# Kernel tuning notes

Hardware: AMD Instinct MI355X
Metric: run time of the kernel (lower is better)

Reference implementation:

```python
import jax, jax.numpy as jnp
import numpy as np
from math import factorial as _fact

# ---- sizes / hyperparams (match init_kwargs) ----
N_NODES, N_EDGES = 8192, 131072
C, H, NRAD, NUM_LAYERS = 64, 64, 8, 2
R_MAX, AVG_NN = 5.0, 16.0
LS = (0, 1, 2)  # irreps degrees carried by node features and edge SH

# ---- real-basis Clebsch-Gordan coefficients (computed once in numpy) ----
def _cg_scalar(j1, m1, j2, m2, j3, m3):
    if m1 + m2 != m3:
        return 0.0
    pre = ((2*j3+1) * _fact(j1+j2-j3) * _fact(j1-j2+j3) * _fact(-j1+j2+j3)
           / _fact(j1+j2+j3+1)) ** 0.5
    pre *= (_fact(j1+m1)*_fact(j1-m1)*_fact(j2+m2)*_fact(j2-m2)
            * _fact(j3+m3)*_fact(j3-m3)) ** 0.5
    s = 0.0
    for k in range(max(0, j2-j3-m1, j1+m2-j3), min(j1+j2-j3, j1-m1, j2+m2)+1):
        s += (-1)**k / (_fact(k)*_fact(j1+j2-j3-k)*_fact(j1-m1-k)
                        * _fact(j2+m2-k)*_fact(j3-j2+m1+k)*_fact(j3-j1-m2+k))
    return pre * s

def _U_real(l):
    # unitary: Y_real = U @ Y_complex, components ordered m=-l..l
    U = np.zeros((2*l+1, 2*l+1), dtype=complex)
    s2 = 2 ** -0.5
    for m in range(-l, l+1):
        if m > 0:
            U[m+l, m+l] = (-1)**m * s2
            U[m+l, -m+l] = s2
        elif m == 0:
            U[l, l] = 1.0
        else:
            U[m+l, m+l] = 1j*s2
            U[m+l, -m+l] = -1j*(-1)**(-m)*s2
    return U

def _real_cg(l1, l2, l3):
    Cc = np.zeros((2*l1+1, 2*l2+1, 2*l3+1))
    for i1, m1 in enumerate(range(-l1, l1+1)):
        for i2, m2 in enumerate(range(-l2, l2+1)):
            m3 = m1 + m2
            if abs(m3) <= l3:
                Cc[i1, i2, m3+l3] = _cg_scalar(l1, m1, l2, m2, l3, m3)
    U1, U2, U3 = _U_real(l1), _U_real(l2), _U_real(l3)
    W = np.einsum('ia,jb,kc,abc->ijk', U1.conj(), U2.conj(), U3, Cc.astype(complex))
    W = W.real if np.linalg.norm(W.real) >= np.linalg.norm(W.imag) else W.imag
    W = W / np.linalg.norm(W) * (2*l3+1) ** 0.5  # component-style normalization
    return jnp.asarray(W, dtype=jnp.float32)

PATHS = [(l1, l2, l3) for l1 in LS for l2 in LS for l3 in LS
         if abs(l1 - l2) <= l3 <= l1 + l2]  # 15 tensor-product paths
CGS = [_real_cg(*p) for p in PATHS]
N_PATHS = len(PATHS)


def _sph(u):
    # real spherical harmonics of unit vectors, l=0,1,2, m=-l..l ordering
    x, y, z = u[:, 0], u[:, 1], u[:, 2]
    sh0 = jnp.ones((u.shape[0], 1), u.dtype)
    sh1 = jnp.sqrt(3.0) * jnp.stack([y, z, x], axis=-1)
    sh2 = jnp.stack([jnp.sqrt(15.0)*x*y, jnp.sqrt(15.0)*y*z,
                     jnp.sqrt(5.0)/2*(3*z*z - 1.0),
                     jnp.sqrt(15.0)*x*z, jnp.sqrt(15.0)/2*(x*x - y*y)], axis=-1)
    return (sh0, sh1, sh2)


def _forward(positions, embed, w_proj, mlp_w1, mlp_b1, mlp_w2, mlp_b2, mlp_w3,
             lin_self, gate_w, gate_b, species, senders, receivers):
    n = positions.shape[0]
    rel = (positions[receivers] - positions[senders]) / R_MAX  # [E,3]
    d = jnp.linalg.norm(rel, axis=-1)                          # [E]
    u = rel / jnp.maximum(d, 1e-6)[:, None]
    sh = _sph(u)
    freqs = jnp.arange(1, NRAD + 1, dtype=positions.dtype)
    xr = jnp.clip(d, 1e-4, 1.0)[:, None]
    basis = jnp.sqrt(2.0) * jnp.sin(freqs * jnp.pi * xr) / xr  # Bessel [E,NRAD]
    cut = 0.5 * (jnp.cos(jnp.pi * jnp.clip(d, 0.0, 1.0)) + 1.0)  # smooth cutoff

    # initial species embedding -> scalar (0e) features; l>0 start at zero
    x0 = embed[species] @ w_proj                                # [N,C]
    feats = [x0[:, :, None],
             jnp.zeros((n, C, 3), x0.dtype),
             jnp.zeros((n, C, 5), x0.dtype)]

    inv_sqrt_nn = 1.0 / jnp.sqrt(jnp.asarray(AVG_NN, x0.dtype))
    for i in range(NUM_LAYERS):
        # radial MLP -> per-path, per-channel edge weights
        h = jax.nn.silu(basis @ mlp_w1[i] + mlp_b1[i])
        h = jax.nn.silu(h @ mlp_w2[i] + mlp_b2[i])
        w = (h @ mlp_w3[i]).reshape(-1, N_PATHS, C) * cut[:, None, None]
        xg = [feats[l][senders] for l in LS]                    # edge gather
        msgs = [0.0, 0.0, 0.0]
        for p, (l1, l2, l3) in enumerate(PATHS):
            m = jnp.einsum('eci,ej,ijk->eck', xg[l1], sh[l2], CGS[p])
            msgs[l3] = msgs[l3] + m * w[:, p, :, None]
        agg = [jax.ops.segment_sum(msgs[l], receivers, num_segments=n) * inv_sqrt_nn
               for l in LS]
        # self-interaction linears + gated nonlinearity + skip
        y = [jnp.einsum('ncm,cd->ndm', agg[l], lin_self[i, l]) for l in LS]
        feats[0] = feats[0] + jax.nn.silu(y[0])
        g_in = feats[0][:, :, 0]                                # [N,C] scalars
        for l in (1, 2):
            g = jax.nn.sigmoid(g_in @ gate_w[i, l-1] + gate_b[i, l-1])
            feats[l] = feats[l] + g[:, :, None] * y[l]

    # alpha = 0.5 ** l per irrep, then flatten to [N, C*(1+3+5)]
    return jnp.concatenate([(feats[l] * (0.5 ** l)).reshape(n, -1) for l in LS],
                           axis=-1)


def setup_inputs() -> dict:
    key = jax.random.key(0)
    ks = jax.random.split(key, 12)
    f32 = jnp.float32
    return {
        'positions': jax.random.normal(ks[0], (N_NODES, 3), f32),
        'species': jax.random.randint(ks[1], (N_NODES,), 0, 5),
        'senders': jax.random.randint(ks[2], (N_EDGES,), 0, N_NODES),
        'receivers': jax.random.randint(ks[3], (N_EDGES,), 0, N_NODES),
        'embed': jax.random.normal(ks[4], (5, 32), f32),
        'w_proj': jax.random.normal(ks[5], (32, C), f32) / jnp.sqrt(32.0),
        'mlp_w1': jax.random.normal(ks[6], (NUM_LAYERS, NRAD, H), f32) / jnp.sqrt(float(NRAD)),
        'mlp_b1': jnp.zeros((NUM_LAYERS, H), f32),
        'mlp_w2': jax.random.normal(ks[7], (NUM_LAYERS, H, H), f32) / jnp.sqrt(float(H)),
        'mlp_b2': jnp.zeros((NUM_LAYERS, H), f32),
        'mlp_w3': jax.random.normal(ks[8], (NUM_LAYERS, H, N_PATHS * C), f32) / jnp.sqrt(float(H)),
        'lin_self': jax.random.normal(ks[9], (NUM_LAYERS, 3, C, C), f32) / jnp.sqrt(float(C)),
        'gate_w': jax.random.normal(ks[10], (NUM_LAYERS, 2, C, C), f32) / jnp.sqrt(float(C)),
        'gate_b': jnp.zeros((NUM_LAYERS, 2, C), f32),
    }


def reference(positions, species, senders, receivers, embed, w_proj, mlp_w1,
              mlp_b1, mlp_w2, mlp_b2, mlp_w3, lin_self, gate_w, gate_b):
    return _forward(positions, embed, w_proj, mlp_w1, mlp_b1, mlp_w2, mlp_b2,
                    mlp_w3, lin_self, gate_w, gate_b, species, senders, receivers)
```

## Files before the change

kernel.cpp:

```cpp
#include <hip/hip_runtime.h>
#include <cmath>
#include <algorithm>

#define N_NODES 8192
#define N_EDGES 131072
#define NPATHS 15
#define FPN 576
#define NODE_BLK 16
#define SWROW 968

typedef unsigned short ushortx;
typedef unsigned int uintx;
typedef short short8 __attribute__((ext_vector_type(8)));
typedef float f32x4 __attribute__((ext_vector_type(4)));

constexpr int PL1[NPATHS] = {0,0,0,1,1,1,1,1,1,2,2,2,2,2,2};
constexpr int PL2[NPATHS] = {0,1,2,0,1,1,1,2,2,0,1,1,2,2,2};
constexpr int PL3[NPATHS] = {0,1,2,1,0,1,2,1,2,2,1,2,0,1,2};
constexpr int CGOFF[NPATHS] = {0,1,10,35,44,53,80,125,170,245,270,315,390,415,490};
constexpr int CGTOT = 615;
constexpr int BOFF[3] = {0,1,4};

struct CGTable { float v[CGTOT]; };

namespace cgb {
struct C2 { double re, im; };
static inline C2 cmul(C2 a, C2 b){ return {a.re*b.re - a.im*b.im, a.re*b.im + a.im*b.re}; }
static double factd(int n){ double r=1.0; for (int i=2;i<=n;++i) r*=i; return r; }

static double cg_scalar(int j1,int m1,int j2,int m2,int j3,int m3){
  if (m1+m2 != m3) return 0.0;
  double pre = std::sqrt((2.0*j3+1.0)*factd(j1+j2-j3)*factd(j1-j2+j3)*factd(-j1+j2+j3)/factd(j1+j2+j3+1));
  pre *= std::sqrt(factd(j1+m1)*factd(j1-m1)*factd(j2+m2)*factd(j2-m2)*factd(j3+m3)*factd(j3-m3));
  double s = 0.0;
  int kmin = std::max(0, std::max(j2-j3-m1, j1+m2-j3));
  int kmax = std::min(j1+j2-j3, std::min(j1-m1, j2+m2));
  for (int k=kmin;k<=kmax;++k){
    double t = 1.0/(factd(k)*factd(j1+j2-j3-k)*factd(j1-m1-k)*factd(j2+m2-k)*factd(j3-j2+m1+k)*factd(j3-j1-m2+k));
    s += (k&1) ? -t : t;
  }
  return pre*s;
}

static void makeU(int l, C2 U[5][5]){
  double s2 = std::sqrt(0.5);
  for (int a=0;a<5;++a) for (int b=0;b<5;++b) U[a][b] = {0.0,0.0};
  for (int m=-l;m<=l;++m){
    if (m > 0){
      U[m+l][ m+l] = {((m&1)?-1.0:1.0)*s2, 0.0};
      U[m+l][-m+l] = {s2, 0.0};
    } else if (m == 0){
      U[l][l] = {1.0, 0.0};
    } else {
      U[m+l][ m+l] = {0.0, s2};
      U[m+l][-m+l] = {0.0, -((((-m)&1))?-1.0:1.0)*s2};
    }
  }
}
}

static CGTable build_cg_table(){
  using namespace cgb;
  CGTable t{};
  for (int p=0;p<NPATHS;++p){
    int l1=PL1[p], l2=PL2[p], l3=PL3[p];
    int n1=2*l1+1, n2=2*l2+1, n3=2*l3+1;
    double Cc[5][5][5] = {};
    for (int i1=0;i1<n1;++i1) for (int i2=0;i2<n2;++i2){
      int m1=i1-l1, m2=i2-l2, m3=m1+m2;
      if (m3 >= -l3 && m3 <= l3) Cc[i1][i2][m3+l3] = cg_scalar(l1,m1,l2,m2,l3,m3);
    }
    C2 U1[5][5], U2[5][5], U3[5][5];
    makeU(l1,U1); makeU(l2,U2); makeU(l3,U3);
    double Wre[5][5][5]={}, Wim[5][5][5]={};
    for (int i=0;i<n1;++i) for (int j=0;j<n2;++j) for (int k=0;k<n3;++k){
      double are=0.0, aim=0.0;
      for (int a=0;a<n1;++a) for (int b=0;b<n2;++b){
        int m3 = (a-l1)+(b-l2);
        if (m3 < -l3 || m3 > l3) continue;
        double cv = Cc[a][b][m3+l3];
        if (cv == 0.0) continue;
        C2 u1c = {U1[i][a].re, -U1[i][a].im};
        C2 u2c = {U2[j][b].re, -U2[j][b].im};
        C2 tt = cmul(cmul(u1c, u2c), U3[k][m3+l3]);
        are += tt.re*cv; aim += tt.im*cv;
      }
      Wre[i][j][k]=are; Wim[i][j][k]=aim;
    }
    double nr=0.0, ni=0.0;
    for (int i=0;i<n1;++i) for (int j=0;j<n2;++j) for (int k=0;k<n3;++k){
      nr += Wre[i][j][k]*Wre[i][j][k]; ni += Wim[i][j][k]*Wim[i][j][k];
    }
    bool useRe = std::sqrt(nr) >= std::sqrt(ni);
    double nrm = std::sqrt(useRe ? nr : ni);
    double scale = std::sqrt((double)n3) / nrm;
    for (int i=0;i<n1;++i) for (int j=0;j<n2;++j) for (int k=0;k<n3;++k)
      t.v[CGOFF[p] + (i*n2+j)*n3 + k] =
        (float)((useRe ? Wre[i][j][k] : Wim[i][j][k]) * scale);
  }
  return t;
}

static const CGTable& cg_table(){ static CGTable t = build_cg_table(); return t; }

__device__ __forceinline__ float siluf(float x){ return x / (1.0f + expf(-x)); }
__device__ __forceinline__ float sigmf(float x){ return 1.0f / (1.0f + expf(-x)); }
__device__ __forceinline__ ushortx f2b(float f){
  uintx u = __float_as_uint(f);
  u += 0x7fffu + ((u >> 16) & 1u);
  return (ushortx)(u >> 16);
}
__device__ __forceinline__ float b2f(ushortx b){ return __uint_as_float(((uintx)b) << 16); }

__global__ __launch_bounds__(64) void k_init(const int* __restrict__ species,
    const float* __restrict__ embed, const float* __restrict__ wproj,
    float* __restrict__ feats)
{
  const int n = blockIdx.x, c = threadIdx.x;
  const int sp = species[n];
  float acc = 0.f;
  #pragma unroll
  for (int q=0;q<32;++q) acc += embed[sp*32+q]*wproj[q*64+c];
  feats[n*FPN + c] = acc;
  #pragma unroll
  for (int j=0;j<8;++j) feats[n*FPN + 64 + j*64 + c] = 0.f;
}

__global__ __launch_bounds__(256) void k_out(const float* __restrict__ feats,
                                             float* __restrict__ out)
{
  const int n = blockIdx.x;
  for (int j = threadIdx.x; j < FPN; j += 256){
    float sc = (j < 64) ? 1.0f : ((j < 256) ? 0.5f : 0.25f);
    out[n*FPN + j] = feats[n*FPN + j] * sc;
  }
}

__global__ __launch_bounds__(256) void k_hist(const int* __restrict__ receivers,
                                              int* __restrict__ cnt)
{
  int e = blockIdx.x*256 + threadIdx.x;
  atomicAdd(&cnt[receivers[e]], 1);
}

__global__ __launch_bounds__(1024) void k_scan(const int* __restrict__ cnt,
    int* __restrict__ row_start, int* __restrict__ cursor)
{
  __shared__ int part[1024];
  const int t = threadIdx.x;
  int loc[8];
  #pragma unroll
  for (int i=0;i<8;++i) loc[i] = cnt[t*8+i];
  int sum = 0;
  #pragma unroll
  for (int i=0;i<8;++i) sum += loc[i];
  part[t] = sum;
  __syncthreads();
  for (int off=1; off<1024; off<<=1){
    int x = (t >= off) ? part[t-off] : 0;
    __syncthreads();
    part[t] += x;
    __syncthreads();
  }
  int run = (t > 0) ? part[t-1] : 0;
  #pragma unroll
  for (int i=0;i<8;++i){
    row_start[t*8+i] = run;
    cursor[t*8+i]    = run;
    run += loc[i];
  }
  if (t == 1023) row_start[8192] = run;
}

__global__ __launch_bounds__(256) void k_scatter(const int* __restrict__ receivers,
    int* __restrict__ cursor, int* __restrict__ perm)
{
  int e = blockIdx.x*256 + threadIdx.x;
  int r = receivers[e];
  int pos = atomicAdd(&cursor[r], 1);
  perm[pos] = e;
}

__global__ __launch_bounds__(256) void k_geom(const float* __restrict__ pos,
    const int* __restrict__ senders, const int* __restrict__ receivers,
    const int* __restrict__ perm,
    float* __restrict__ sh8s, float* __restrict__ d_s,
    int* __restrict__ send_s, int* __restrict__ recv_s)
{
  const int i = blockIdx.x*256 + threadIdx.x;
  const int e = perm[i];
  const int s = senders[e], r = receivers[e];
  send_s[i] = s;
  recv_s[i] = r;
  float rx = (pos[r*3+0] - pos[s*3+0]) * 0.2f;
  float ry = (pos[r*3+1] - pos[s*3+1]) * 0.2f;
  float rz = (pos[r*3+2] - pos[s*3+2]) * 0.2f;
  float d  = sqrtf(rx*rx + ry*ry + rz*rz);
  d_s[i] = d;
  float iv = 1.0f / fmaxf(d, 1e-6f);
  float x = rx*iv, y = ry*iv, z = rz*iv;
  const float s3   = 1.7320508075688772f;
  const float s15  = 3.8729833462074170f;
  const float s5h  = 1.1180339887498949f;
  const float s15h = 1.9364916731037085f;
  sh8s[i*8+0] = s3*y;
  sh8s[i*8+1] = s3*z;
  sh8s[i*8+2] = s3*x;
  sh8s[i*8+3] = s15*x*y;
  sh8s[i*8+4] = s15*y*z;
  sh8s[i*8+5] = s5h*(3.f*z*z - 1.f);
  sh8s[i*8+6] = s15*x*z;
  sh8s[i*8+7] = s15h*(x*x - y*y);
}

__global__ __launch_bounds__(256) void k_mlp(
    const float* __restrict__ d_s,
    const float* __restrict__ w1, const float* __restrict__ b1,
    const float* __restrict__ w2, const float* __restrict__ b2,
    ushortx* __restrict__ h2p)
{
  __shared__ float s_w2[4096];
  __shared__ float s_h1[4*64];
  const int tid = threadIdx.x, wv = tid>>6, lane = tid&63;
  const float PI = 3.14159265358979323846f;
  for (int i=tid;i<4096;i+=256) s_w2[i] = w2[i];
  __syncthreads();
  #pragma unroll
  for (int ee=0; ee<2; ++ee){
    const int i = blockIdx.x*8 + wv*2 + ee;
    const float d = d_s[i];
    float xr = fminf(fmaxf(d, 1e-4f), 1.0f);
    float ixr = 1.0f/xr;
    float acc = b1[lane];
    #pragma unroll
    for (int q=0;q<8;++q){
      float bs = 1.4142135623730951f * sinf((float)(q+1)*PI*xr) * ixr;
      acc = fmaf(bs, w1[q*64+lane], acc);
    }
    s_h1[wv*64+lane] = siluf(acc);
    __syncthreads();
    float acc2 = b2[lane];
    #pragma unroll
    for (int k=0;k<64;++k) acc2 = fmaf(s_h1[wv*64+k], s_w2[k*64+lane], acc2);
    float dc = fminf(fmaxf(d, 0.f), 1.f);
    float cut = 0.5f*(cosf(PI*dc) + 1.f);
    float h2 = siluf(acc2) * cut * 0.25f;
    h2p[(size_t)i*64+lane] = f2b(h2);
    __syncthreads();
  }
}

__global__ __launch_bounds__(256) void k_w3t(const float* __restrict__ w3,
                                             ushortx* __restrict__ w3t)
{
  int g = blockIdx.x*256 + threadIdx.x;
  int n = g >> 6, k = g & 63;
  w3t[g] = f2b(w3[k*960 + n]);
}

__global__ __launch_bounds__(256) void k_aggmm(
    const float* __restrict__ featsIn, float* __restrict__ featsOut,
    const ushortx* __restrict__ h2p, const ushortx* __restrict__ w3t,
    const float* __restrict__ sh8s, const int* __restrict__ send_s,
    const int* __restrict__ recv_s, const int* __restrict__ rowst,
    const float* __restrict__ lin, const float* __restrict__ gw,
    const float* __restrict__ gb, const CGTable cg)
{
  __shared__ float   s_agg[NODE_BLK*FPN];
  __shared__ ushortx s_w[16*SWROW];
  __shared__ ushortx s_a[16*72];

  const int tid  = threadIdx.x;
  const int wv   = tid >> 6;
  const int lane = tid & 63;
  const int n0   = blockIdx.x * NODE_BLK;
  const int beg  = rowst[n0];
  const int end  = rowst[n0 + NODE_BLK];

  for (int k = tid; k < NODE_BLK*FPN; k += 256) s_agg[k] = 0.f;
  __syncthreads();

  const int q = lane >> 4, mrow = lane & 15;

  for (int ebeg = beg; ebeg < end; ebeg += 16){
    {
      int er = tid >> 4, seg = tid & 15;
      int i = ebeg + er;
      if (i >= end) i = end - 1;
      *(uint2*)&s_a[er*72 + seg*4] =
        *(const uint2*)&h2p[(size_t)i*64 + seg*4];
    }
    __syncthreads();

    short8 a0 = *(const short8*)&s_a[mrow*72 +      q*8];
    short8 a1 = *(const short8*)&s_a[mrow*72 + 32 + q*8];
    #pragma unroll
    for (int nt=0; nt<15; ++nt){
      const int col = wv*240 + nt*16 + mrow;
      short8 b0 = *(const short8*)&w3t[(size_t)col*64 +      q*8];
      short8 b1 = *(const short8*)&w3t[(size_t)col*64 + 32 + q*8];
      f32x4 acc = {0.f,0.f,0.f,0.f};
      acc = __builtin_amdgcn_mfma_f32_16x16x32_bf16(a0, b0, acc, 0, 0, 0);
      acc = __builtin_amdgcn_mfma_f32_16x16x32_bf16(a1, b1, acc, 0, 0, 0);
      #pragma unroll
      for (int r=0;r<4;++r)
        s_w[(q*4+r)*SWROW + col] = f2b(acc[r]);
    }
    __syncthreads();

    #pragma unroll
    for (int ee=0; ee<4; ++ee){
      const int slot = wv*4 + ee;
      const int i = ebeg + slot;
      if (i < end){
        const int s  = send_s[i];
        const int rl = recv_s[i] - n0;
        const float* fb = featsIn + (size_t)s*FPN;
        float X[9];
        X[0] = fb[lane];
        #pragma unroll
        for (int mm=0;mm<3;++mm) X[1+mm] = fb[64  + lane*3 + mm];
        #pragma unroll
        for (int mm=0;mm<5;++mm) X[4+mm] = fb[256 + lane*5 + mm];
        float S[9];
        S[0] = 1.f;
        #pragma unroll
        for (int j=0;j<8;++j) S[1+j] = sh8s[(size_t)i*8+j];
        float w[NPATHS];
        #pragma unroll
        for (int p=0;p<NPATHS;++p) w[p] = b2f(s_w[slot*SWROW + p*64 + lane]);
        float m[9];
        #pragma unroll
        for (int k=0;k<9;++k) m[k] = 0.f;
        #pragma unroll
        for (int p=0;p<NPATHS;++p){
          const int l1=PL1[p], l2=PL2[p], l3=PL3[p];
          const int n2=2*l2+1, n3=2*l3+1;
          const float wp_ = w[p];
          #pragma unroll
          for (int ii=0;ii<2*l1+1;++ii){
            #pragma unroll
            for (int jj=0;jj<n2;++jj){
              float t = wp_ * X[BOFF[l1]+ii] * S[BOFF[l2]+jj];
              #pragma unroll
              for (int k=0;k<n3;++k)
                m[BOFF[l3]+k] = fmaf(cg.v[CGOFF[p] + (ii*n2+jj)*n3 + k], t, m[BOFF[l3]+k]);
            }
          }
        }
        float* ab = s_agg + rl*FPN;
        atomicAdd(&ab[lane], m[0]);
        #pragma unroll
        for (int mm=0;mm<3;++mm) atomicAdd(&ab[64  + lane*3 + mm], m[1+mm]);
        #pragma unroll
        for (int mm=0;mm<5;++mm) atomicAdd(&ab[256 + lane*5 + mm], m[4+mm]);
      }
    }
    __syncthreads();
  }

  #pragma unroll
  for (int k=0;k<4;++k){
    const int ln = wv*4 + k;
    const int n  = n0 + ln;
    const float* ag = s_agg + ln*FPN;
    float y[9];
    #pragma unroll
    for (int j=0;j<9;++j) y[j] = 0.f;
    for (int c=0;c<64;++c){
      float l0 = lin[          c*64 + lane];
      float l1 = lin[4096    + c*64 + lane];
      float l2 = lin[8192    + c*64 + lane];
      y[0] = fmaf(ag[c], l0, y[0]);
      #pragma unroll
      for (int mm=0;mm<3;++mm) y[1+mm] = fmaf(ag[64  + c*3 + mm], l1, y[1+mm]);
      #pragma unroll
      for (int mm=0;mm<5;++mm) y[4+mm] = fmaf(ag[256 + c*5 + mm], l2, y[4+mm]);
    }
    const size_t base = (size_t)n*FPN;
    float f0 = featsIn[base + lane] + siluf(y[0]);
    featsOut[base + lane] = f0;
    float a1 = gb[lane], a2 = gb[64 + lane];
    for (int c=0;c<64;++c){
      float fc = __shfl(f0, c);
      a1 = fmaf(fc, gw[        c*64 + lane], a1);
      a2 = fmaf(fc, gw[4096 +  c*64 + lane], a2);
    }
    float g1 = sigmf(a1), g2 = sigmf(a2);
    #pragma unroll
    for (int mm=0;mm<3;++mm)
      featsOut[base + 64  + lane*3 + mm] = featsIn[base + 64  + lane*3 + mm] + g1*y[1+mm];
    #pragma unroll
    for (int mm=0;mm<5;++mm)
      featsOut[base + 256 + lane*5 + mm] = featsIn[base + 256 + lane*5 + mm] + g2*y[4+mm];
  }
}

__global__ __launch_bounds__(256) void k_edge_fb(
    const float* __restrict__ pos,
    const int* __restrict__ senders, const int* __restrict__ receivers,
    const float* __restrict__ w1, const float* __restrict__ b1,
    const float* __restrict__ w2, const float* __restrict__ b2,
    const float* __restrict__ w3,
    const float* __restrict__ feats, float* __restrict__ agg,
    const CGTable cg)
{
  __shared__ float s_h1[16*64];
  __shared__ float s_h2[16*64];
  __shared__ float s_w3[8*960];
  __shared__ float s_sh[16][8];
  __shared__ float s_cut[16];

  const int tid  = threadIdx.x;
  const int wave = tid >> 6;
  const int lane = tid & 63;
  const int ebase = blockIdx.x * 16;
  const float PI = 3.14159265358979323846f;

  #pragma unroll
  for (int ee=0; ee<4; ++ee){
    const int slot = wave*4 + ee;
    const int e = ebase + slot;
    const int s = senders[e], r = receivers[e];
    float rx = (pos[r*3+0] - pos[s*3+0]) * 0.2f;
    float ry = (pos[r*3+1] - pos[s*3+1]) * 0.2f;
    float rz = (pos[r*3+2] - pos[s*3+2]) * 0.2f;
    float d  = sqrtf(rx*rx + ry*ry + rz*rz);
    float iv = 1.0f / fmaxf(d, 1e-6f);
    float x = rx*iv, y = ry*iv, z = rz*iv;
    if (lane == 0){
      const float s3   = 1.7320508075688772f;
      const float s15  = 3.8729833462074170f;
      const float s5h  = 1.1180339887498949f;
      const float s15h = 1.9364916731037085f;
      s_sh[slot][0] = s3*y;  s_sh[slot][1] = s3*z;  s_sh[slot][2] = s3*x;
      s_sh[slot][3] = s15*x*y; s_sh[slot][4] = s15*y*z;
      s_sh[slot][5] = s5h*(3.f*z*z - 1.f);
      s_sh[slot][6] = s15*x*z; s_sh[slot][7] = s15h*(x*x - y*y);
      float dc = fminf(fmaxf(d, 0.f), 1.f);
      s_cut[slot] = 0.5f*(cosf(PI*dc) + 1.f);
    }
    float xr = fminf(fmaxf(d, 1e-4f), 1.0f);
    float ixr = 1.0f/xr;
    float acc = b1[lane];
    #pragma unroll
    for (int q=0;q<8;++q)
      acc += 1.4142135623730951f * sinf((float)(q+1)*PI*xr) * ixr * w1[q*64 + lane];
    s_h1[slot*64 + lane] = siluf(acc);
  }
  __syncthreads();
  #pragma unroll
  for (int ee=0; ee<4; ++ee){
    const int slot = wave*4 + ee;
    float acc = b2[lane];
    #pragma unroll
    for (int k=0;k<64;++k) acc += s_h1[slot*64+k] * w2[k*64+lane];
    s_h2[slot*64+lane] = siluf(acc);
  }
  __syncthreads();

  float wgt[NPATHS][4];
  #pragma unroll
  for (int p=0;p<NPATHS;++p){ wgt[p][0]=wgt[p][1]=wgt[p][2]=wgt[p][3]=0.f; }
  for (int kc=0;kc<8;++kc){
    #pragma unroll
    for (int rr=0;rr<8;++rr){
      #pragma unroll
      for (int jj=0;jj<4;++jj){
        int col = jj*256 + tid;
        if (col < 960) s_w3[rr*960+col] = w3[(kc*8+rr)*960+col];
      }
    }
    __syncthreads();
    #pragma unroll
    for (int kk=0;kk<8;++kk){
      float h2v[4];
      #pragma unroll
      for (int ee=0;ee<4;++ee) h2v[ee] = s_h2[(wave*4+ee)*64 + kc*8+kk];
      #pragma unroll
      for (int p=0;p<NPATHS;++p){
        float wv = s_w3[kk*960 + p*64 + lane];
        #pragma unroll
        for (int ee=0;ee<4;++ee) wgt[p][ee] = fmaf(h2v[ee], wv, wgt[p][ee]);
      }
    }
    __syncthreads();
  }
  #pragma unroll
  for (int ee=0;ee<4;++ee){
    float f = s_cut[wave*4+ee] * 0.25f;
    #pragma unroll
    for (int p=0;p<NPATHS;++p) wgt[p][ee] *= f;
  }
  #pragma unroll
  for (int ee=0;ee<4;++ee){
    const int slot = wave*4 + ee;
    const int e = ebase + slot;
    const int s = senders[e];
    const int r = receivers[e];
    const int sb = s*FPN;
    float X[9], S[9], msg[9];
    X[0] = feats[sb + lane];
    #pragma unroll
    for (int mm=0;mm<3;++mm) X[1+mm] = feats[sb + 64  + lane*3 + mm];
    #pragma unroll
    for (int mm=0;mm<5;++mm) X[4+mm] = feats[sb + 256 + lane*5 + mm];
    S[0] = 1.f;
    #pragma unroll
    for (int j=0;j<8;++j) S[1+j] = s_sh[slot][j];
    #pragma unroll
    for (int k=0;k<9;++k) msg[k] = 0.f;
    #pragma unroll
    for (int p=0;p<NPATHS;++p){
      const int l1=PL1[p], l2=PL2[p], l3=PL3[p];
      const int n2=2*l2+1, n3=2*l3+1;
      const float wp = wgt[p][ee];
      #pragma unroll
      for (int i=0;i<2*l1+1;++i){
        #pragma unroll
        for (int j=0;j<n2;++j){
          float t = wp * X[BOFF[l1]+i] * S[BOFF[l2]+j];
          #pragma unroll
          for (int k=0;k<n3;++k)
            msg[BOFF[l3]+k] = fmaf(cg.v[CGOFF[p] + (i*n2+j)*n3 + k], t, msg[BOFF[l3]+k]);
        }
      }
    }
    const int rb = r*FPN;
    unsafeAtomicAdd(&agg[rb + lane], msg[0]);
    #pragma unroll
    for (int mm=0;mm<3;++mm) unsafeAtomicAdd(&agg[rb + 64  + lane*3 + mm], msg[1+mm]);
    #pragma unroll
    for (int mm=0;mm<5;++mm) unsafeAtomicAdd(&agg[rb + 256 + lane*5 + mm], msg[4+mm]);
  }
}

__global__ __launch_bounds__(64) void k_node_fb(
    float* __restrict__ feats, const float* __restrict__ agg,
    const float* __restrict__ lin, const float* __restrict__ gw,
    const float* __restrict__ gb)
{
  __shared__ float sf0[64];
  const int n = blockIdx.x, d = threadIdx.x;
  const int base = n*FPN;
  float y[9];
  #pragma unroll
  for (int k=0;k<9;++k) y[k]=0.f;
  for (int c=0;c<64;++c){
    float l0 = lin[          c*64 + d];
    float l1 = lin[4096    + c*64 + d];
    float l2 = lin[8192    + c*64 + d];
    y[0] = fmaf(agg[base + c], l0, y[0]);
    #pragma unroll
    for (int mm=0;mm<3;++mm) y[1+mm] = fmaf(agg[base + 64  + c*3 + mm], l1, y[1+mm]);
    #pragma unroll
    for (int mm=0;mm<5;++mm) y[4+mm] = fmaf(agg[base + 256 + c*5 + mm], l2, y[4+mm]);
  }
  float f0 = feats[base + d] + siluf(y[0]);
  feats[base + d] = f0;
  sf0[d] = f0;
  __syncthreads();
  {
    float acc = gb[d];
    for (int c=0;c<64;++c) acc = fmaf(sf0[c], gw[c*64 + d], acc);
    float g = sigmf(acc);
    #pragma unroll
    for (int mm=0;mm<3;++mm) feats[base + 64 + d*3 + mm] += g*y[1+mm];
  }
  {
    float acc = gb[64 + d];
    for (int c=0;c<64;++c) acc = fmaf(sf0[c], gw[4096 + c*64 + d], acc);
    float g = sigmf(acc);
    #pragma unroll
    for (int mm=0;mm<5;++mm) feats[base + 256 + d*5 + mm] += g*y[4+mm];
  }
}

extern "C" void kernel_launch(void* const* d_in, const int* in_sizes, int n_in,
                              void* d_out, int out_size, void* d_ws, size_t ws_size,
                              hipStream_t stream)
{
  const float* pos      = (const float*)d_in[0];
  const int*   species  = (const int*)  d_in[1];
  const int*   senders  = (const int*)  d_in[2];
  const int*   receivers= (const int*)  d_in[3];
  const float* embed    = (const float*)d_in[4];
  const float* wproj    = (const float*)d_in[5];
  const float* w1       = (const float*)d_in[6];
  const float* b1       = (const float*)d_in[7];
  const float* w2       = (const float*)d_in[8];
  const float* b2       = (const float*)d_in[9];
  const float* w3       = (const float*)d_in[10];
  const float* lin      = (const float*)d_in[11];
  const float* gw       = (const float*)d_in[12];
  const float* gb       = (const float*)d_in[13];

  const CGTable& cg = cg_table();

  char* p = (char*)d_ws;
  size_t off = 0;
  auto alloc = [&](size_t bytes)->char*{
    char* r = p + off;
    off += (bytes + 255) & ~(size_t)255;
    return r;
  };
  float*   featsA = (float*)  alloc((size_t)N_NODES*FPN*4);
  float*   featsB = (float*)  alloc((size_t)N_NODES*FPN*4);
  int*     cnt    = (int*)    alloc(N_NODES*4);
  int*     cursor = (int*)    alloc(N_NODES*4);
  int*     rowst  = (int*)    alloc((N_NODES+1)*4);
  int*     perm   = (int*)    alloc((size_t)N_EDGES*4);
  int*     send_s = (int*)    alloc((size_t)N_EDGES*4);
  int*     recv_s = (int*)    alloc((size_t)N_EDGES*4);
  float*   d_sArr = (float*)  alloc((size_t)N_EDGES*4);
  float*   sh8s   = (float*)  alloc((size_t)N_EDGES*8*4);
  ushortx* h2p    = (ushortx*)alloc((size_t)N_EDGES*64*2);
  ushortx* w3t    = (ushortx*)alloc((size_t)960*64*2);
  const size_t need_main = off;

  if (ws_size >= need_main){
    hipMemsetAsync(cnt, 0, N_NODES*4, stream);
    hipLaunchKernelGGL(k_hist,    dim3(N_EDGES/256), dim3(256), 0, stream, receivers, cnt);
    hipLaunchKernelGGL(k_scan,    dim3(1), dim3(1024), 0, stream, cnt, rowst, cursor);
    hipLaunchKernelGGL(k_scatter, dim3(N_EDGES/256), dim3(256), 0, stream, receivers, cursor, perm);
    hipLaunchKernelGGL(k_geom,    dim3(N_EDGES/256), dim3(256), 0, stream,
                       pos, senders, receivers, perm, sh8s, d_sArr, send_s, recv_s);
    hipLaunchKernelGGL(k_init,    dim3(N_NODES), dim3(64), 0, stream,
                       species, embed, wproj, featsA);
    for (int L=0; L<2; ++L){
      const float* fin  = (L == 0) ? featsA : featsB;
      float*       fout = (L == 0) ? featsB : featsA;
      hipLaunchKernelGGL(k_mlp,  dim3(N_EDGES/8), dim3(256), 0, stream,
                         d_sArr, w1 + L*512, b1 + L*64, w2 + L*4096, b2 + L*64, h2p);
      hipLaunchKernelGGL(k_w3t,  dim3(240), dim3(256), 0, stream, w3 + (size_t)L*61440, w3t);
      hipLaunchKernelGGL(k_aggmm, dim3(N_NODES/NODE_BLK), dim3(256), 0, stream,
                         fin, fout, h2p, w3t, sh8s, send_s, recv_s, rowst,
                         lin + L*3*64*64, gw + L*2*64*64, gb + L*2*64, cg);
    }
    hipLaunchKernelGGL(k_out, dim3(N_NODES), dim3(256), 0, stream, featsA, (float*)d_out);
  } else {
    float* feats = (float*)d_ws;
    float* agg   = feats + (size_t)N_NODES*FPN;
    hipLaunchKernelGGL(k_init, dim3(N_NODES), dim3(64), 0, stream,
                       species, embed, wproj, feats);
    for (int L=0; L<2; ++L){
      hipMemsetAsync(agg, 0, (size_t)N_NODES*FPN*sizeof(float), stream);
      hipLaunchKernelGGL(k_edge_fb, dim3(N_EDGES/16), dim3(256), 0, stream,
                         pos, senders, receivers,
                         w1 + L*512, b1 + L*64, w2 + L*4096, b2 + L*64,
                         w3 + (size_t)L*61440, feats, agg, cg);
      hipLaunchKernelGGL(k_node_fb, dim3(N_NODES), dim3(64), 0, stream,
                         feats, agg, lin + L*3*64*64, gw + L*2*64*64, gb + L*2*64);
    }
    hipLaunchKernelGGL(k_out, dim3(N_NODES), dim3(256), 0, stream, feats, (float*)d_out);
  }
}
```

Baseline: 1.730 ms.

## Halve node block and split edge-weight MMA by channel halves to cut LDS use

The aggregation kernel now processes 8 nodes per block instead of 16, and computes the per-edge path weights in two channel halves so the shared weight buffer is halved. Each wave handles two edges at once with 32 channels per half-wave. Launch bounds request 4 blocks per SM. The aim is lower LDS and register footprint, which allows more resident blocks and more parallelism over nodes. The cost is an extra synchronisation per edge batch and more blocks redoing per-block setup.

```diff
diff --git a/kernel.cpp b/kernel.cpp
--- a/kernel.cpp
+++ b/kernel.cpp
@@ -6,8 +6,8 @@
 #define N_EDGES 131072
 #define NPATHS 15
 #define FPN 576
-#define NODE_BLK 16
-#define SWROW 968
+#define NODE_BLK 8
+#define SWROW 488
 
 typedef unsigned short ushortx;
 typedef unsigned int uintx;
@@ -258,7 +258,7 @@
   w3t[g] = f2b(w3[k*960 + n]);
 }
 
-__global__ __launch_bounds__(256) void k_aggmm(
+__global__ __launch_bounds__(256,4) void k_aggmm(
     const float* __restrict__ featsIn, float* __restrict__ featsOut,
     const ushortx* __restrict__ h2p, const ushortx* __restrict__ w3t,
     const float* __restrict__ sh8s, const int* __restrict__ send_s,
@@ -281,6 +281,8 @@
   __syncthreads();
 
   const int q = lane >> 4, mrow = lane & 15;
+  const int ch_lo = lane & 31;
+  const int epar  = lane >> 5;
 
   for (int ebeg = beg; ebeg < end; ebeg += 16){
     {
@@ -294,74 +296,84 @@
 
     short8 a0 = *(const short8*)&s_a[mrow*72 +      q*8];
     short8 a1 = *(const short8*)&s_a[mrow*72 + 32 + q*8];
-    #pragma unroll
-    for (int nt=0; nt<15; ++nt){
-      const int col = wv*240 + nt*16 + mrow;
-      short8 b0 = *(const short8*)&w3t[(size_t)col*64 +      q*8];
-      short8 b1 = *(const short8*)&w3t[(size_t)col*64 + 32 + q*8];
-      f32x4 acc = {0.f,0.f,0.f,0.f};
-      acc = __builtin_amdgcn_mfma_f32_16x16x32_bf16(a0, b0, acc, 0, 0, 0);
-      acc = __builtin_amdgcn_mfma_f32_16x16x32_bf16(a1, b1, acc, 0, 0, 0);
-      #pragma unroll
-      for (int r=0;r<4;++r)
-        s_w[(q*4+r)*SWROW + col] = f2b(acc[r]);
-    }
-    __syncthreads();
-
-    #pragma unroll
-    for (int ee=0; ee<4; ++ee){
-      const int slot = wv*4 + ee;
-      const int i = ebeg + slot;
-      if (i < end){
-        const int s  = send_s[i];
-        const int rl = recv_s[i] - n0;
-        const float* fb = featsIn + (size_t)s*FPN;
-        float X[9];
-        X[0] = fb[lane];
-        #pragma unroll
-        for (int mm=0;mm<3;++mm) X[1+mm] = fb[64  + lane*3 + mm];
-        #pragma unroll
-        for (int mm=0;mm<5;++mm) X[4+mm] = fb[256 + lane*5 + mm];
-        float S[9];
-        S[0] = 1.f;
-        #pragma unroll
-        for (int j=0;j<8;++j) S[1+j] = sh8s[(size_t)i*8+j];
-        float w[NPATHS];
-        #pragma unroll
-        for (int p=0;p<NPATHS;++p) w[p] = b2f(s_w[slot*SWROW + p*64 + lane]);
-        float m[9];
-        #pragma unroll
-        for (int k=0;k<9;++k) m[k] = 0.f;
-        #pragma unroll
-        for (int p=0;p<NPATHS;++p){
-          const int l1=PL1[p], l2=PL2[p], l3=PL3[p];
-          const int n2=2*l2+1, n3=2*l3+1;
-          const float wp_ = w[p];
-          #pragma unroll
-          for (int ii=0;ii<2*l1+1;++ii){
+
+    #pragma unroll
+    for (int h=0; h<2; ++h){
+      #pragma unroll
+      for (int t=0; t<8; ++t){
+        const int j = wv + 4*t;
+        if (j < 30){
+          const int pth = j >> 1, sub = j & 1;
+          const int gc  = pth*64 + h*32 + sub*16 + mrow;
+          short8 b0 = *(const short8*)&w3t[(size_t)gc*64 +      q*8];
+          short8 b1 = *(const short8*)&w3t[(size_t)gc*64 + 32 + q*8];
+          f32x4 acc = {0.f,0.f,0.f,0.f};
+          acc = __builtin_amdgcn_mfma_f32_16x16x32_bf16(a0, b0, acc, 0, 0, 0);
+          acc = __builtin_amdgcn_mfma_f32_16x16x32_bf16(a1, b1, acc, 0, 0, 0);
+          const int lc = pth*32 + sub*16 + mrow;
+          #pragma unroll
+          for (int r=0;r<4;++r)
+            s_w[(q*4+r)*SWROW + lc] = f2b(acc[r]);
+        }
+      }
+      __syncthreads();
+
+      #pragma unroll
+      for (int pair=0; pair<2; ++pair){
+        const int slot = wv*4 + pair*2 + epar;
+        const int i = ebeg + slot;
+        if (i < end){
+          const int ch = h*32 + ch_lo;
+          const int s  = send_s[i];
+          const int rl = recv_s[i] - n0;
+          const float* fb = featsIn + (size_t)s*FPN;
+          float X[9];
+          X[0] = fb[ch];
+          #pragma unroll
+          for (int mm=0;mm<3;++mm) X[1+mm] = fb[64  + ch*3 + mm];
+          #pragma unroll
+          for (int mm=0;mm<5;++mm) X[4+mm] = fb[256 + ch*5 + mm];
+          float S[9];
+          S[0] = 1.f;
+          #pragma unroll
+          for (int jj=0;jj<8;++jj) S[1+jj] = sh8s[(size_t)i*8+jj];
+          float w[NPATHS];
+          #pragma unroll
+          for (int p=0;p<NPATHS;++p) w[p] = b2f(s_w[slot*SWROW + p*32 + ch_lo]);
+          float m[9];
+          #pragma unroll
+          for (int k=0;k<9;++k) m[k] = 0.f;
+          #pragma unroll
+          for (int p=0;p<NPATHS;++p){
+            const int l1=PL1[p], l2=PL2[p], l3=PL3[p];
+            const int n2=2*l2+1, n3=2*l3+1;
+            const float wp_ = w[p];
             #pragma unroll
-            for (int jj=0;jj<n2;++jj){
-              float t = wp_ * X[BOFF[l1]+ii] * S[BOFF[l2]+jj];
+            for (int ii=0;ii<2*l1+1;++ii){
               #pragma unroll
-              for (int k=0;k<n3;++k)
-                m[BOFF[l3]+k] = fmaf(cg.v[CGOFF[p] + (ii*n2+jj)*n3 + k], t, m[BOFF[l3]+k]);
+              for (int jj=0;jj<n2;++jj){
+                float t = wp_ * X[BOFF[l1]+ii] * S[BOFF[l2]+jj];
+                #pragma unroll
+                for (int k=0;k<n3;++k)
+                  m[BOFF[l3]+k] = fmaf(cg.v[CGOFF[p] + (ii*n2+jj)*n3 + k], t, m[BOFF[l3]+k]);
+              }
             }
           }
+          float* ab = s_agg + rl*FPN;
+          atomicAdd(&ab[ch], m[0]);
+          #pragma unroll
+          for (int mm=0;mm<3;++mm) atomicAdd(&ab[64  + ch*3 + mm], m[1+mm]);
+          #pragma unroll
+          for (int mm=0;mm<5;++mm) atomicAdd(&ab[256 + ch*5 + mm], m[4+mm]);
         }
-        float* ab = s_agg + rl*FPN;
-        atomicAdd(&ab[lane], m[0]);
-        #pragma unroll
-        for (int mm=0;mm<3;++mm) atomicAdd(&ab[64  + lane*3 + mm], m[1+mm]);
-        #pragma unroll
-        for (int mm=0;mm<5;++mm) atomicAdd(&ab[256 + lane*5 + mm], m[4+mm]);
       }
-    }
-    __syncthreads();
-  }
-
-  #pragma unroll
-  for (int k=0;k<4;++k){
-    const int ln = wv*4 + k;
+      __syncthreads();
+    }
+  }
+
+  #pragma unroll
+  for (int k=0;k<2;++k){
+    const int ln = wv*2 + k;
     const int n  = n0 + ln;
     const float* ag = s_agg + ln*FPN;
     float y[9];
```

Result: slower. 1.791 ms (+3.5%).

## Use bf16 component-major node features, register run-accumulation, smaller node blocks

Applied to the files above, without the earlier changes.

Node features are now stored component-major, as fp32 master state plus a bf16 gather copy. This halves the bytes moved by the per-edge sender gather and makes those loads coalesced. Messages for consecutive edges that share a receiver are summed in registers, so the LDS atomics are flushed only when the receiver changes. NODE_BLK drops from 16 to 8 and the kernel gets a 3-block occupancy hint, giving more blocks and more waves in flight. The cost is bf16 precision on gathered features, an extra bf16 buffer to write, and a transpose in the output kernel.

```diff
diff --git a/kernel.cpp b/kernel.cpp
--- a/kernel.cpp
+++ b/kernel.cpp
@@ -6,7 +6,7 @@
 #define N_EDGES 131072
 #define NPATHS 15
 #define FPN 576
-#define NODE_BLK 16
+#define NODE_BLK 8
 #define SWROW 968
 
 typedef unsigned short ushortx;
@@ -114,7 +114,7 @@
 
 __global__ __launch_bounds__(64) void k_init(const int* __restrict__ species,
     const float* __restrict__ embed, const float* __restrict__ wproj,
-    float* __restrict__ feats)
+    float* __restrict__ feats, ushortx* __restrict__ featsG)
 {
   const int n = blockIdx.x, c = threadIdx.x;
   const int sp = species[n];
@@ -122,18 +122,25 @@
   #pragma unroll
   for (int q=0;q<32;++q) acc += embed[sp*32+q]*wproj[q*64+c];
   feats[n*FPN + c] = acc;
-  #pragma unroll
-  for (int j=0;j<8;++j) feats[n*FPN + 64 + j*64 + c] = 0.f;
-}
-
-__global__ __launch_bounds__(256) void k_out(const float* __restrict__ feats,
-                                             float* __restrict__ out)
-{
-  const int n = blockIdx.x;
-  for (int j = threadIdx.x; j < FPN; j += 256){
-    float sc = (j < 64) ? 1.0f : ((j < 256) ? 0.5f : 0.25f);
-    out[n*FPN + j] = feats[n*FPN + j] * sc;
-  }
+  featsG[n*FPN + c] = f2b(acc);
+  #pragma unroll
+  for (int r=1;r<9;++r){
+    feats[n*FPN + r*64 + c] = 0.f;
+    featsG[n*FPN + r*64 + c] = 0;
+  }
+}
+
+__global__ __launch_bounds__(64) void k_out_t(const float* __restrict__ feats,
+                                              float* __restrict__ out)
+{
+  const int n = blockIdx.x, c = threadIdx.x;
+  const float* f = feats + (size_t)n*FPN;
+  float* o = out + (size_t)n*FPN;
+  o[c] = f[c];
+  #pragma unroll
+  for (int mm=0;mm<3;++mm) o[64 + c*3 + mm] = f[(1+mm)*64 + c] * 0.5f;
+  #pragma unroll
+  for (int mm=0;mm<5;++mm) o[256 + c*5 + mm] = f[(4+mm)*64 + c] * 0.25f;
 }
 
 __global__ __launch_bounds__(256) void k_hist(const int* __restrict__ receivers,
@@ -258,8 +265,9 @@
   w3t[g] = f2b(w3[k*960 + n]);
 }
 
-__global__ __launch_bounds__(256) void k_aggmm(
-    const float* __restrict__ featsIn, float* __restrict__ featsOut,
+__global__ __launch_bounds__(256,3) void k_aggmm(
+    float* __restrict__ feats,
+    const ushortx* __restrict__ featsGin, ushortx* __restrict__ featsGout,
     const ushortx* __restrict__ h2p, const ushortx* __restrict__ w3t,
     const float* __restrict__ sh8s, const int* __restrict__ send_s,
     const int* __restrict__ recv_s, const int* __restrict__ rowst,
@@ -281,6 +289,11 @@
   __syncthreads();
 
   const int q = lane >> 4, mrow = lane & 15;
+
+  float macc[9];
+  #pragma unroll
+  for (int k=0;k<9;++k) macc[k] = 0.f;
+  int cur_rl = -1;
 
   for (int ebeg = beg; ebeg < end; ebeg += 16){
     {
@@ -315,23 +328,20 @@
       if (i < end){
         const int s  = send_s[i];
         const int rl = recv_s[i] - n0;
-        const float* fb = featsIn + (size_t)s*FPN;
+        const ushortx* fg = featsGin + (size_t)s*FPN;
         float X[9];
-        X[0] = fb[lane];
         #pragma unroll
-        for (int mm=0;mm<3;++mm) X[1+mm] = fb[64  + lane*3 + mm];
-        #pragma unroll
-        for (int mm=0;mm<5;++mm) X[4+mm] = fb[256 + lane*5 + mm];
+        for (int r=0;r<9;++r) X[r] = b2f(fg[r*64 + lane]);
         float S[9];
         S[0] = 1.f;
         #pragma unroll
-        for (int j=0;j<8;++j) S[1+j] = sh8s[(size_t)i*8+j];
+        for (int jj=0;jj<8;++jj) S[1+jj] = sh8s[(size_t)i*8+jj];
         float w[NPATHS];
         #pragma unroll
         for (int p=0;p<NPATHS;++p) w[p] = b2f(s_w[slot*SWROW + p*64 + lane]);
-        float m[9];
+        float mloc[9];
         #pragma unroll
-        for (int k=0;k<9;++k) m[k] = 0.f;
+        for (int k=0;k<9;++k) mloc[k] = 0.f;
         #pragma unroll
         for (int p=0;p<NPATHS;++p){
           const int l1=PL1[p], l2=PL2[p], l3=PL3[p];
@@ -344,24 +354,38 @@
               float t = wp_ * X[BOFF[l1]+ii] * S[BOFF[l2]+jj];
               #pragma unroll
               for (int k=0;k<n3;++k)
-                m[BOFF[l3]+k] = fmaf(cg.v[CGOFF[p] + (ii*n2+jj)*n3 + k], t, m[BOFF[l3]+k]);
+                mloc[BOFF[l3]+k] = fmaf(cg.v[CGOFF[p] + (ii*n2+jj)*n3 + k], t, mloc[BOFF[l3]+k]);
             }
           }
         }
-        float* ab = s_agg + rl*FPN;
-        atomicAdd(&ab[lane], m[0]);
-        #pragma unroll
-        for (int mm=0;mm<3;++mm) atomicAdd(&ab[64  + lane*3 + mm], m[1+mm]);
-        #pragma unroll
-        for (int mm=0;mm<5;++mm) atomicAdd(&ab[256 + lane*5 + mm], m[4+mm]);
+        if (rl != cur_rl){
+          if (cur_rl >= 0){
+            float* ab = s_agg + cur_rl*FPN;
+            #pragma unroll
+            for (int r=0;r<9;++r) atomicAdd(&ab[r*64 + lane], macc[r]);
+          }
+          cur_rl = rl;
+          #pragma unroll
+          for (int k=0;k<9;++k) macc[k] = mloc[k];
+        } else {
+          #pragma unroll
+          for (int k=0;k<9;++k) macc[k] += mloc[k];
+        }
       }
     }
     __syncthreads();
   }
 
-  #pragma unroll
-  for (int k=0;k<4;++k){
-    const int ln = wv*4 + k;
+  if (cur_rl >= 0){
+    float* ab = s_agg + cur_rl*FPN;
+    #pragma unroll
+    for (int r=0;r<9;++r) atomicAdd(&ab[r*64 + lane], macc[r]);
+  }
+  __syncthreads();
+
+  #pragma unroll
+  for (int k=0;k<2;++k){
+    const int ln = wv*2 + k;
     const int n  = n0 + ln;
     const float* ag = s_agg + ln*FPN;
     float y[9];
@@ -373,13 +397,14 @@
       float l2 = lin[8192    + c*64 + lane];
       y[0] = fmaf(ag[c], l0, y[0]);
       #pragma unroll
-      for (int mm=0;mm<3;++mm) y[1+mm] = fmaf(ag[64  + c*3 + mm], l1, y[1+mm]);
+      for (int mm=0;mm<3;++mm) y[1+mm] = fmaf(ag[(1+mm)*64 + c], l1, y[1+mm]);
       #pragma unroll
-      for (int mm=0;mm<5;++mm) y[4+mm] = fmaf(ag[256 + c*5 + mm], l2, y[4+mm]);
+      for (int mm=0;mm<5;++mm) y[4+mm] = fmaf(ag[(4+mm)*64 + c], l2, y[4+mm]);
     }
     const size_t base = (size_t)n*FPN;
-    float f0 = featsIn[base + lane] + siluf(y[0]);
-    featsOut[base + lane] = f0;
+    float f0 = feats[base + lane] + siluf(y[0]);
+    feats[base + lane] = f0;
+    featsGout[base + lane] = f2b(f0);
     float a1 = gb[lane], a2 = gb[64 + lane];
     for (int c=0;c<64;++c){
       float fc = __shfl(f0, c);
@@ -388,11 +413,41 @@
     }
     float g1 = sigmf(a1), g2 = sigmf(a2);
     #pragma unroll
-    for (int mm=0;mm<3;++mm)
-      featsOut[base + 64  + lane*3 + mm] = featsIn[base + 64  + lane*3 + mm] + g1*y[1+mm];
-    #pragma unroll
-    for (int mm=0;mm<5;++mm)
-      featsOut[base + 256 + lane*5 + mm] = featsIn[base + 256 + lane*5 + mm] + g2*y[4+mm];
+    for (int mm=0;mm<3;++mm){
+      float v = feats[base + (1+mm)*64 + lane] + g1*y[1+mm];
+      feats[base + (1+mm)*64 + lane] = v;
+      featsGout[base + (1+mm)*64 + lane] = f2b(v);
+    }
+    #pragma unroll
+    for (int mm=0;mm<5;++mm){
+      float v = feats[base + (4+mm)*64 + lane] + g2*y[4+mm];
+      feats[base + (4+mm)*64 + lane] = v;
+      featsGout[base + (4+mm)*64 + lane] = f2b(v);
+    }
+  }
+}
+
+__global__ __launch_bounds__(64) void k_init_fb(const int* __restrict__ species,
+    const float* __restrict__ embed, const float* __restrict__ wproj,
+    float* __restrict__ feats)
+{
+  const int n = blockIdx.x, c = threadIdx.x;
+  const int sp = species[n];
+  float acc = 0.f;
+  #pragma unroll
+  for (int q=0;q<32;++q) acc += embed[sp*32+q]*wproj[q*64+c];
+  feats[n*FPN + c] = acc;
+  #pragma unroll
+  for (int j=0;j<8;++j) feats[n*FPN + 64 + j*64 + c] = 0.f;
+}
+
+__global__ __launch_bounds__(256) void k_out_fb(const float* __restrict__ feats,
+                                                float* __restrict__ out)
+{
+  const int n = blockIdx.x;
+  for (int j = threadIdx.x; j < FPN; j += 256){
+    float sc = (j < 64) ? 1.0f : ((j < 256) ? 0.5f : 0.25f);
+    out[n*FPN + j] = feats[n*FPN + j] * sc;
   }
 }
 
@@ -604,18 +659,19 @@
     off += (bytes + 255) & ~(size_t)255;
     return r;
   };
-  float*   featsA = (float*)  alloc((size_t)N_NODES*FPN*4);
-  float*   featsB = (float*)  alloc((size_t)N_NODES*FPN*4);
-  int*     cnt    = (int*)    alloc(N_NODES*4);
-  int*     cursor = (int*)    alloc(N_NODES*4);
-  int*     rowst  = (int*)    alloc((N_NODES+1)*4);
-  int*     perm   = (int*)    alloc((size_t)N_EDGES*4);
-  int*     send_s = (int*)    alloc((size_t)N_EDGES*4);
-  int*     recv_s = (int*)    alloc((size_t)N_EDGES*4);
-  float*   d_sArr = (float*)  alloc((size_t)N_EDGES*4);
-  float*   sh8s   = (float*)  alloc((size_t)N_EDGES*8*4);
-  ushortx* h2p    = (ushortx*)alloc((size_t)N_EDGES*64*2);
-  ushortx* w3t    = (ushortx*)alloc((size_t)960*64*2);
+  float*   featsA  = (float*)  alloc((size_t)N_NODES*FPN*4);
+  ushortx* featsGA = (ushortx*)alloc((size_t)N_NODES*FPN*2);
+  ushortx* featsGB = (ushortx*)alloc((size_t)N_NODES*FPN*2);
+  int*     cnt     = (int*)    alloc(N_NODES*4);
+  int*     cursor  = (int*)    alloc(N_NODES*4);
+  int*     rowst   = (int*)    alloc((N_NODES+1)*4);
+  int*     perm    = (int*)    alloc((size_t)N_EDGES*4);
+  int*     send_s  = (int*)    alloc((size_t)N_EDGES*4);
+  int*     recv_s  = (int*)    alloc((size_t)N_EDGES*4);
+  float*   d_sArr  = (float*)  alloc((size_t)N_EDGES*4);
+  float*   sh8s    = (float*)  alloc((size_t)N_EDGES*8*4);
+  ushortx* h2p     = (ushortx*)alloc((size_t)N_EDGES*64*2);
+  ushortx* w3t     = (ushortx*)alloc((size_t)960*64*2);
   const size_t need_main = off;
 
   if (ws_size >= need_main){
@@ -626,22 +682,22 @@
     hipLaunchKernelGGL(k_geom,    dim3(N_EDGES/256), dim3(256), 0, stream,
                        pos, senders, receivers, perm, sh8s, d_sArr, send_s, recv_s);
     hipLaunchKernelGGL(k_init,    dim3(N_NODES), dim3(64), 0, stream,
-                       species, embed, wproj, featsA);
+                       species, embed, wproj, featsA, featsGA);
     for (int L=0; L<2; ++L){
-      const float* fin  = (L == 0) ? featsA : featsB;
-      float*       fout = (L == 0) ? featsB : featsA;
+      const ushortx* gin  = (L == 0) ? featsGA : featsGB;
+      ushortx*       gout = (L == 0) ? featsGB : featsGA;
       hipLaunchKernelGGL(k_mlp,  dim3(N_EDGES/8), dim3(256), 0, stream,
                          d_sArr, w1 + L*512, b1 + L*64, w2 + L*4096, b2 + L*64, h2p);
       hipLaunchKernelGGL(k_w3t,  dim3(240), dim3(256), 0, stream, w3 + (size_t)L*61440, w3t);
       hipLaunchKernelGGL(k_aggmm, dim3(N_NODES/NODE_BLK), dim3(256), 0, stream,
-                         fin, fout, h2p, w3t, sh8s, send_s, recv_s, rowst,
+                         featsA, gin, gout, h2p, w3t, sh8s, send_s, recv_s, rowst,
                          lin + L*3*64*64, gw + L*2*64*64, gb + L*2*64, cg);
     }
-    hipLaunchKernelGGL(k_out, dim3(N_NODES), dim3(256), 0, stream, featsA, (float*)d_out);
+    hipLaunchKernelGGL(k_out_t, dim3(N_NODES), dim3(64), 0, stream, featsA, (float*)d_out);
   } else {
     float* feats = (float*)d_ws;
     float* agg   = feats + (size_t)N_NODES*FPN;
-    hipLaunchKernelGGL(k_init, dim3(N_NODES), dim3(64), 0, stream,
+    hipLaunchKernelGGL(k_init_fb, dim3(N_NODES), dim3(64), 0, stream,
                        species, embed, wproj, feats);
     for (int L=0; L<2; ++L){
       hipMemsetAsync(agg, 0, (size_t)N_NODES*FPN*sizeof(float), stream);
@@ -652,6 +708,6 @@
       hipLaunchKernelGGL(k_node_fb, dim3(N_NODES), dim3(64), 0, stream,
                          feats, agg, lin + L*3*64*64, gw + L*2*64*64, gb + L*2*64);
     }
-    hipLaunchKernelGGL(k_out, dim3(N_NODES), dim3(256), 0, stream, feats, (float*)d_out);
-  }
-}
+    hipLaunchKernelGGL(k_out_fb, dim3(N_NODES), dim3(256), 0, stream, feats, (float*)d_out);
+  }
+}
```

Measured after the change: 2.644 ms. 52.8% more time.
